# Optimization experiments

Hardware: AMD Instinct MI355X
Metric: run time of the kernel (lower is better)

Reference implementation:

```python
import jax, jax.numpy as jnp
import numpy as np

B, S, H = 2, 4096, 1024
NKH, NVH, DK, DV = 8, 16, 64, 64
KEY_DIM = NKH * DK
VAL_DIM = NVH * DV
CONV_DIM = 2 * KEY_DIM + VAL_DIM
KSZ = 4
EPS = 1e-6


def setup_inputs() -> dict:
    key = jax.random.key(0)
    ks = jax.random.split(key, 8)
    s = 0.02
    return {
        "hidden_states": jax.random.normal(ks[0], (B, S, H), jnp.float32),
        "W_qkv": jax.random.normal(ks[1], (CONV_DIM, H), jnp.float32) * s,
        "conv_w": jax.random.normal(ks[2], (CONV_DIM, 1, KSZ), jnp.float32) * 0.1,
        "W_z": jax.random.normal(ks[3], (VAL_DIM, H), jnp.float32) * s,
        "W_b": jax.random.normal(ks[4], (NVH, H), jnp.float32) * s,
        "W_a": jax.random.normal(ks[5], (NVH, H), jnp.float32) * s,
        "dt_bias": jnp.ones((NVH,), jnp.float32),
        "A_log": jnp.log(jax.random.uniform(ks[6], (NVH,), jnp.float32, 0.1, 16.0)),
        "norm_weight": jnp.ones((DV,), jnp.float32),
        "W_out": jax.random.normal(ks[7], (H, VAL_DIM), jnp.float32) * s,
    }


def _forward(hidden_states, W_qkv, conv_w, W_z, W_b, W_a, dt_bias, A_log, norm_weight, W_out):
    b, s, _ = hidden_states.shape
    # fused qkv projection -> depthwise causal conv -> silu
    mixed = hidden_states @ W_qkv.T                       # [b,s,conv_dim]
    x = mixed.transpose(0, 2, 1)                          # [b,conv_dim,s]
    y = jax.lax.conv_general_dilated(
        x, conv_w, (1,), [(KSZ - 1, 0)],
        dimension_numbers=("NCH", "OIH", "NCH"),
        feature_group_count=CONV_DIM)                     # causal: left pad k-1
    mixed = jax.nn.silu(y).transpose(0, 2, 1)             # [b,s,conv_dim]

    z = (hidden_states @ W_z.T).reshape(b, s, NVH, DV)
    beta = jax.nn.sigmoid(hidden_states @ W_b.T)          # [b,s,nvh]
    a = hidden_states @ W_a.T
    g = -jnp.exp(A_log) * jax.nn.softplus(a + dt_bias)    # [b,s,nvh]

    q, k, v = jnp.split(mixed, [KEY_DIM, 2 * KEY_DIM], axis=-1)
    q = q.reshape(b, s, NKH, DK)
    k = k.reshape(b, s, NKH, DK)
    v = v.reshape(b, s, NVH, DV)
    rep = NVH // NKH
    if rep > 1:  # GQA: repeat_interleave along head dim
        q = jnp.repeat(q, rep, axis=2)
        k = jnp.repeat(k, rep, axis=2)
    q = q * (DK ** -0.5)

    # gated delta-rule recurrence over time (state: [b,h,dk,dv])
    def step(Sst, inp):
        q_t, k_t, v_t, g_t, b_t = inp                     # [b,h,dk],[b,h,dk],[b,h,dv],[b,h],[b,h]
        Sst = Sst * jnp.exp(g_t)[..., None, None]
        kv = jnp.einsum("bhkv,bhk->bhv", Sst, k_t)
        delta = (v_t - kv) * b_t[..., None]
        Sst = Sst + k_t[..., None] * delta[..., None, :]
        o = jnp.einsum("bhkv,bhk->bhv", Sst, q_t)
        return Sst, o

    S0 = jnp.zeros((b, NVH, DK, DV), jnp.float32)
    xs = (q.transpose(1, 0, 2, 3), k.transpose(1, 0, 2, 3), v.transpose(1, 0, 2, 3),
          g.transpose(1, 0, 2), beta.transpose(1, 0, 2))
    _, o = jax.lax.scan(step, S0, xs)                     # o: [s,b,h,dv]
    o = o.transpose(1, 0, 2, 3)                           # [b,s,h,dv]

    # gated RMSNorm over head_v_dim: x * silu(z), rmsnorm, * weight
    h_ = o * jax.nn.silu(z)
    var = jnp.mean(h_ * h_, axis=-1, keepdims=True)
    h_ = h_ * jax.lax.rsqrt(var + EPS) * norm_weight

    return h_.reshape(b, s, VAL_DIM) @ W_out.T            # [b,s,hidden]


def reference(hidden_states, W_qkv, conv_w, W_z, W_b, W_a, dt_bias, A_log, norm_weight, W_out):
    return _forward(hidden_states, W_qkv, conv_w, W_z, W_b, W_a, dt_bias, A_log, norm_weight, W_out)
```

## Files before the change

### kernel.cpp

```cpp
#include <hip/hip_runtime.h>
#include <hip/hip_bf16.h>
#include <stdint.h>

#define B_    2
#define S_    4096
#define H_    1024
#define NKH_  8
#define NVH_  16
#define DK_   64
#define DV_   64
#define KEYD_ 512
#define CDIM_ 2048
#define VALD_ 1024
#define NCHUNK_ 64
#define CS_   64

using bf16 = __hip_bfloat16;
using bf16x8 = __attribute__((ext_vector_type(8))) short;
using f32x4  = __attribute__((ext_vector_type(4))) float;

__device__ inline float bsh2f(short s) {
  union { ushort u; bf16 h; } c; c.u = (ushort)s; return __bfloat162float(c.h);
}
__device__ inline short f2bsh(float f) {
  union { ushort u; bf16 h; } c; c.h = __float2bfloat16(f); return (short)c.u;
}

__device__ __forceinline__ void gload16(const bf16* g, short* lds) {
  __builtin_amdgcn_global_load_lds(
      (const __attribute__((address_space(1))) void*)g,
      (__attribute__((address_space(3))) void*)lds, 16, 0, 0);
}

__global__ __launch_bounds__(256) void castf2b(const float* __restrict__ x,
                                               bf16* __restrict__ y, long n) {
  const long i = ((long)blockIdx.x * 256 + threadIdx.x) * 4;
  if (i >= n) return;
  float4 v = *(const float4*)(x + i);
  union { ushort4 u; bf16 h[4]; } o;
  o.h[0] = __float2bfloat16(v.x);
  o.h[1] = __float2bfloat16(v.y);
  o.h[2] = __float2bfloat16(v.z);
  o.h[3] = __float2bfloat16(v.w);
  *(ushort4*)(y + i) = o.u;
}

template <typename OT>
__global__ __launch_bounds__(256) void gemm_bt(const bf16* __restrict__ A,
                                               const bf16* __restrict__ Bm,
                                               OT* __restrict__ C,
                                               int M, int N, int K) {
  __shared__ short Asm[128 * 32];
  __shared__ short Bsm[128 * 32];
  const int t = threadIdx.x;
  const int w = t >> 6, l = t & 63;
  const int ntn = N >> 7;
  const int bm = blockIdx.x / ntn, bn = blockIdx.x % ntn;
  const int m0 = bm << 7, n0 = bn << 7;
  const int wm = (w >> 1) << 6, wn = (w & 1) << 6;

  f32x4 acc[4][4] = {};

  const int grow = l >> 2;
  const int gc8 = (l & 3) << 3;
  const bf16* Agl = A + (long)m0 * K + gc8;
  const bf16* Bgl = Bm + (long)n0 * K + gc8;

  const int lm = l & 15;
  const int kk = (l >> 4) << 3;
  const short* ar0 = &Asm[(wm + lm) * 32 + kk];
  const short* br0 = &Bsm[(wn + lm) * 32 + kk];

  for (int k0 = 0; k0 < K; k0 += 32) {
    __syncthreads();
#pragma unroll
    for (int j = 0; j < 2; ++j) {
      const int s = w * 2 + j;
      gload16(Agl + (long)(s * 16 + grow) * K + k0, &Asm[s * 16 * 32]);
      gload16(Bgl + (long)(s * 16 + grow) * K + k0, &Bsm[s * 16 * 32]);
    }
    __syncthreads();
    bf16x8 af[4], bfr[4];
#pragma unroll
    for (int mi = 0; mi < 4; ++mi) af[mi] = *(const bf16x8*)(ar0 + mi * 16 * 32);
#pragma unroll
    for (int ni = 0; ni < 4; ++ni) bfr[ni] = *(const bf16x8*)(br0 + ni * 16 * 32);
#pragma unroll
    for (int mi = 0; mi < 4; ++mi)
#pragma unroll
      for (int ni = 0; ni < 4; ++ni)
        acc[mi][ni] = __builtin_amdgcn_mfma_f32_16x16x32_bf16(af[mi], bfr[ni],
                                                              acc[mi][ni], 0, 0, 0);
  }

  const int r0 = (l >> 4) << 2;
  const int cn = l & 15;
#pragma unroll
  for (int mi = 0; mi < 4; ++mi)
#pragma unroll
    for (int ni = 0; ni < 4; ++ni) {
      long base = (long)(m0 + wm + mi * 16 + r0) * N + (n0 + wn + ni * 16 + cn);
#pragma unroll
      for (int r = 0; r < 4; ++r) {
        if constexpr (sizeof(OT) == 2)
          C[base + (long)r * N] = __float2bfloat16(acc[mi][ni][r]);
        else
          C[base + (long)r * N] = acc[mi][ni][r];
      }
    }
}

__global__ __launch_bounds__(256) void conv3(const bf16* __restrict__ mixed,
                                             const float* __restrict__ cw,
                                             bf16* __restrict__ qkv) {
  const long idx = (long)blockIdx.x * 256 + threadIdx.x;
  const int c0 = (int)(idx & 255) << 3;
  const long row = idx >> 8;
  const int s = (int)(row & (S_ - 1));

  bf16x8 mv[4];
#pragma unroll
  for (int j = 0; j < 4; ++j) {
    if (s - 3 + j >= 0)
      mv[j] = *(const bf16x8*)(mixed + (row + j - 3) * CDIM_ + c0);
    else
      mv[j] = (bf16x8){0, 0, 0, 0, 0, 0, 0, 0};
  }

  const float qs = (c0 < KEYD_) ? 0.125f : 1.f;
  union { ushort4 u4[2]; short h[8]; } o;
#pragma unroll
  for (int e = 0; e < 8; ++e) {
    const float4 w = *(const float4*)(cw + (c0 + e) * 4);
    float acc = 0.f;
    acc = fmaf(w.x, bsh2f(mv[0][e]), acc);
    acc = fmaf(w.y, bsh2f(mv[1][e]), acc);
    acc = fmaf(w.z, bsh2f(mv[2][e]), acc);
    acc = fmaf(w.w, bsh2f(mv[3][e]), acc);
    const float y = qs * (acc / (1.f + __expf(-acc)));
    o.h[e] = f2bsh(y);
  }
  *(bf16x8*)((uint16_t*)qkv + row * CDIM_ + c0) = *(bf16x8*)&o.h[0];
}

__global__ __launch_bounds__(256) void proj_ba2(const float* __restrict__ hs,
                                                const float* __restrict__ Wb,
                                                const float* __restrict__ Wa,
                                                const float* __restrict__ dtb,
                                                const float* __restrict__ Alog,
                                                float* __restrict__ beta,
                                                float* __restrict__ g) {
  __shared__ float4 hrow[8][257];
  const long row0 = (long)blockIdx.x * 8;
  const int tid = threadIdx.x;
  for (int i = tid; i < 2048; i += 256) {
    const int r = i >> 8, c4 = i & 255;
    hrow[r][c4] = *(const float4*)(hs + (row0 + r) * H_ + (long)c4 * 4);
  }
  __syncthreads();
  const int j = tid >> 3, r = tid & 7;
  const float4* Wp = (const float4*)(j < 16 ? Wb + (long)j * H_
                                            : Wa + (long)(j - 16) * H_);
  float4 a4 = {0.f, 0.f, 0.f, 0.f};
#pragma unroll 4
  for (int i = 0; i < 256; ++i) {
    const float4 w = Wp[i];
    const float4 hv = hrow[r][i];
    a4.x = fmaf(w.x, hv.x, a4.x);
    a4.y = fmaf(w.y, hv.y, a4.y);
    a4.z = fmaf(w.z, hv.z, a4.z);
    a4.w = fmaf(w.w, hv.w, a4.w);
  }
  const float acc = (a4.x + a4.y) + (a4.z + a4.w);
  const long row = row0 + r;
  if (j < 16) {
    beta[row * NVH_ + j] = 1.f / (1.f + __expf(-acc));
  } else {
    const int hh = j - 16;
    const float x = acc + dtb[hh];
    const float sp = (x > 20.f) ? x : log1pf(__expf(x));
    g[row * NVH_ + hh] = -__expf(Alog[hh]) * sp;
  }
}

__global__ __launch_bounds__(256) void chunk_pre(const bf16* __restrict__ qkv,
                                                 const float* __restrict__ beta,
                                                 const float* __restrict__ g,
                                                 bf16* __restrict__ Wws,
                                                 bf16* __restrict__ U0ws,
                                                 float* __restrict__ lgws,
                                                 bf16* __restrict__ McT,
                                                 bf16* __restrict__ Bc) {
  __shared__ short Ksm[64][72];
  __shared__ short Vsm[64][72];
  __shared__ float Tsm[64][64];
  __shared__ short KpT[64][72];
  __shared__ float Xl[128][67];
  __shared__ float lgs[64];
  __shared__ float bts[64];
  __shared__ float belg[64];

  short (*XB)[36]   = (short (*)[36]) & Vsm[0][0];
  short (*TloB)[40] = (short (*)[40]) & Ksm[0][0];
  short (*WT)[72]   = (short (*)[72]) & Tsm[0][0];
  short (*U0T)[72]  = Vsm;

  const int blk = blockIdx.x;
  const int hb = blk & 31, c = blk >> 5;
  const long task = (long)hb * 64 + c;
  const int h = hb & 15, b = hb >> 4, kh = h >> 1;
  const long t0 = (long)b * S_ + (long)c * CS_;
  const int tid = threadIdx.x;
  const int wv = tid >> 6, l = tid & 63;
  const int lm = l & 15, lk8 = (l >> 4) << 3;
  const int r0 = (l >> 4) << 2, cn = l & 15;
  const int srow = tid >> 2, scol = (tid & 3) * 16;

  {
    const bf16* kp = qkv + (t0 + srow) * CDIM_ + KEYD_ + kh * 64 + scol;
    const bf16* vp = qkv + (t0 + srow) * CDIM_ + 2 * KEYD_ + h * 64 + scol;
    *(bf16x8*)&Ksm[srow][scol]     = *(const bf16x8*)(kp);
    *(bf16x8*)&Ksm[srow][scol + 8] = *(const bf16x8*)(kp + 8);
    *(bf16x8*)&Vsm[srow][scol]     = *(const bf16x8*)(vp);
    *(bf16x8*)&Vsm[srow][scol + 8] = *(const bf16x8*)(vp + 8);
  }
  if (tid < 64) {
    bts[tid] = beta[(t0 + tid) * NVH_ + h];
    lgs[tid] = g[(t0 + tid) * NVH_ + h];
  }
  __syncthreads();

  if (tid < 64) {
    float x = lgs[tid];
#pragma unroll
    for (int d = 1; d < 64; d <<= 1) {
      const float y = __shfl_up(x, d);
      if (tid >= d) x += y;
    }
    lgs[tid] = x;
    belg[tid] = bts[tid] * __expf(x);
  }
  __syncthreads();

  if (tid < 128) {
    f32x4 acc[2][4] = {};
#pragma unroll
    for (int ks = 0; ks < 2; ++ks) {
      bf16x8 bfr[4];
#pragma unroll
      for (int ni = 0; ni < 4; ++ni)
        bfr[ni] = *(const bf16x8*)&Ksm[ni * 16 + lm][lk8 + ks * 32];
#pragma unroll
      for (int mi = 0; mi < 2; ++mi) {
        bf16x8 afr = *(const bf16x8*)&Ksm[(wv * 2 + mi) * 16 + lm][lk8 + ks * 32];
#pragma unroll
        for (int ni = 0; ni < 4; ++ni)
          acc[mi][ni] = __builtin_amdgcn_mfma_f32_16x16x32_bf16(afr, bfr[ni],
                                                                acc[mi][ni], 0, 0, 0);
      }
    }
#pragma unroll
    for (int mi = 0; mi < 2; ++mi)
#pragma unroll
      for (int ni = 0; ni < 4; ++ni)
#pragma unroll
        for (int r = 0; r < 4; ++r) {
          const int t = (wv * 2 + mi) * 16 + r0 + r;
          const int i = ni * 16 + cn;
          Tsm[t][i] = (i < t) ? bts[t] * __expf(lgs[t] - lgs[i]) * acc[mi][ni][r]
                              : 0.f;
        }
  } else {
    const int idx = tid - 128;
    const int tt = idx >> 1;
    const int o2 = (idx & 1) * 32;
    const float dec = __expf(lgs[63] - lgs[tt]);
#pragma unroll 8
    for (int k = 0; k < 32; ++k)
      KpT[o2 + k][tt] = f2bsh(dec * bsh2f(Ksm[tt][o2 + k]));
  }
  __syncthreads();

  auto solve32 = [&](int base) {
    for (int j = base; j < base + 32; j += 8) {
      float xs[8];
#pragma unroll
      for (int a = 0; a < 8; ++a) xs[a] = Xl[tid][j + a];
#pragma unroll
      for (int a = 1; a < 8; ++a)
#pragma unroll
        for (int bb = 0; bb < a; ++bb)
          xs[a] = fmaf(-Tsm[j + a][j + bb], xs[bb], xs[a]);
#pragma unroll
      for (int a = 1; a < 8; ++a) Xl[tid][j + a] = xs[a];
      const int tend = base + 32;
#pragma unroll 2
      for (int tt = j + 8; tt < tend; ++tt) {
        const float4 ta = *(const float4*)&Tsm[tt][j];
        const float4 tb = *(const float4*)&Tsm[tt][j + 4];
        float v = Xl[tid][tt];
        v = fmaf(-ta.x, xs[0], v); v = fmaf(-ta.y, xs[1], v);
        v = fmaf(-ta.z, xs[2], v); v = fmaf(-ta.w, xs[3], v);
        v = fmaf(-tb.x, xs[4], v); v = fmaf(-tb.y, xs[5], v);
        v = fmaf(-tb.z, xs[6], v); v = fmaf(-tb.w, xs[7], v);
        Xl[tid][tt] = v;
      }
    }
  };

  if (tid < 128) {
    const int colW = tid & 63;
    const bool isW = tid < 64;
#pragma unroll 8
    for (int t = 0; t < CS_; ++t)
      Xl[tid][t] = isW ? belg[t] * bsh2f(Ksm[t][colW])
                       : bts[t] * bsh2f(Vsm[t][colW]);
    solve32(0);
  }
  if (tid < 64) lgws[task * 64 + tid] = lgs[tid];
  __syncthreads();

  {
    const int col = tid & 127, uh = (tid >> 7) * 16;
#pragma unroll
    for (int u = 0; u < 16; ++u)
      XB[col][uh + u] = f2bsh(Xl[col][uh + u]);
  }
  if (tid < 128) {
    const int m = tid >> 2, u0 = (tid & 3) * 8;
#pragma unroll
    for (int u = 0; u < 8; ++u)
      TloB[m][u0 + u] = f2bsh(Tsm[32 + m][u0 + u]);
  }
  __syncthreads();

  {
#pragma unroll
    for (int ni2 = 0; ni2 < 2; ++ni2) {
      const int ni = wv * 2 + ni2;
      bf16x8 bfr = *(const bf16x8*)&XB[ni * 16 + lm][lk8];
#pragma unroll
      for (int mi = 0; mi < 2; ++mi) {
        bf16x8 afr = *(const bf16x8*)&TloB[mi * 16 + lm][lk8];
        f32x4 uacc = {};
        uacc = __builtin_amdgcn_mfma_f32_16x16x32_bf16(afr, bfr, uacc, 0, 0, 0);
#pragma unroll
        for (int r = 0; r < 4; ++r)
          Xl[ni * 16 + cn][32 + mi * 16 + r0 + r] -= uacc[r];
      }
    }
  }
  __syncthreads();

  if (tid < 128) solve32(32);
  __syncthreads();

  if (tid < 128) {
    const int colW = tid & 63;
    const bool isW = tid < 64;
    bf16* dst = (isW ? Wws : U0ws) + task * 4096 + colW;
    short (*XT)[72] = isW ? WT : U0T;
#pragma unroll 4
    for (int t = 0; t < CS_; t += 2) {
      const float v0 = Xl[tid][t], v1 = Xl[tid][t + 1];
      dst[(long)t * 64] = __float2bfloat16(v0);
      dst[(long)(t + 1) * 64] = __float2bfloat16(v1);
      short2 pk; pk.x = f2bsh(v0); pk.y = f2bsh(v1);
      *(short2*)&XT[colW][t] = pk;
    }
  }
  __syncthreads();

  {
    f32x4 macc[4] = {};
#pragma unroll
    for (int ks = 0; ks < 2; ++ks) {
      bf16x8 afr = *(const bf16x8*)&KpT[wv * 16 + lm][lk8 + ks * 32];
#pragma unroll
      for (int ni = 0; ni < 4; ++ni) {
        bf16x8 bfr = *(const bf16x8*)&WT[ni * 16 + lm][lk8 + ks * 32];
        macc[ni] = __builtin_amdgcn_mfma_f32_16x16x32_bf16(afr, bfr, macc[ni], 0, 0, 0);
      }
    }
#pragma unroll
    for (int ni = 0; ni < 4; ++ni)
#pragma unroll
      for (int r = 0; r < 4; ++r)
        McT[task * 4096 + (wv * 16 + r0 + r) * 64 + ni * 16 + cn] =
            __float2bfloat16(-macc[ni][r]);
  }
  {
    f32x4 bacc[4] = {};
#pragma unroll
    for (int ks = 0; ks < 2; ++ks) {
      bf16x8 afr = *(const bf16x8*)&U0T[wv * 16 + lm][lk8 + ks * 32];
#pragma unroll
      for (int ni = 0; ni < 4; ++ni) {
        bf16x8 bfr = *(const bf16x8*)&KpT[ni * 16 + lm][lk8 + ks * 32];
        bacc[ni] = __builtin_amdgcn_mfma_f32_16x16x32_bf16(afr, bfr, bacc[ni], 0, 0, 0);
      }
    }
#pragma unroll
    for (int ni = 0; ni < 4; ++ni)
#pragma unroll
      for (int r = 0; r < 4; ++r)
        Bc[task * 4096 + (wv * 16 + r0 + r) * 64 + ni * 16 + cn] =
            __float2bfloat16(bacc[ni][r]);
  }
}

__global__ __launch_bounds__(256) void chunk_state(const bf16* __restrict__ McT,
                                                   const bf16* __restrict__ Bc,
                                                   const float* __restrict__ lgws,
                                                   bf16* __restrict__ Sb) {
  __shared__ short Msm[2][4][64][72];
  __shared__ short Bsm[2][4][64][72];
  __shared__ short Ssm[64][72];
  __shared__ float lgsm[2][4];

  const int hb = blockIdx.x;
  const int tid = threadIdx.x, wv = tid >> 6, l = tid & 63;
  const int lm = l & 15, lk8 = (l >> 4) << 3;
  const int r0 = (l >> 4) << 2, cn = l & 15;
  const int srow = tid >> 2, scol = (tid & 3) * 16;

  for (int i = tid; i < 64 * 72; i += 256) ((short*)Ssm)[i] = 0;
  f32x4 Sreg[4] = {};

  bf16x8 mr0[4], mr1[4], br0[4], br1[4];
  float lgn0, lgn1, lgn2, lgn3;

  auto gload = [&](int g) {
#pragma unroll
    for (int cc = 0; cc < 4; ++cc) {
      const long tt = (long)hb * 64 + g * 4 + cc;
      const bf16* mp = McT + tt * 4096 + srow * 64 + scol;
      const bf16* bp = Bc + tt * 4096 + srow * 64 + scol;
      mr0[cc] = *(const bf16x8*)(mp);
      mr1[cc] = *(const bf16x8*)(mp + 8);
      br0[cc] = *(const bf16x8*)(bp);
      br1[cc] = *(const bf16x8*)(bp + 8);
    }
    const long tb = (long)hb * 64 + g * 4;
    lgn0 = lgws[(tb + 0) * 64 + 63];
    lgn1 = lgws[(tb + 1) * 64 + 63];
    lgn2 = lgws[(tb + 2) * 64 + 63];
    lgn3 = lgws[(tb + 3) * 64 + 63];
  };
  auto lwrite = [&](int g) {
    const int bu = g & 1;
#pragma unroll
    for (int cc = 0; cc < 4; ++cc) {
      *(bf16x8*)&Msm[bu][cc][srow][scol]     = mr0[cc];
      *(bf16x8*)&Msm[bu][cc][srow][scol + 8] = mr1[cc];
      *(bf16x8*)&Bsm[bu][cc][srow][scol]     = br0[cc];
      *(bf16x8*)&Bsm[bu][cc][srow][scol + 8] = br1[cc];
    }
    if (tid == 0) {
      lgsm[bu][0] = lgn0; lgsm[bu][1] = lgn1;
      lgsm[bu][2] = lgn2; lgsm[bu][3] = lgn3;
    }
  };

  gload(0);
  lwrite(0);
  gload(1);
  __syncthreads();

  for (int g = 0; g < 16; ++g) {
    const int bu = g & 1;
    if (g + 1 < 16) lwrite(g + 1);
    if (g + 2 < 16) gload(g + 2);
#pragma unroll
    for (int cc = 0; cc < 4; ++cc) {
      const int c = g * 4 + cc;
      {
        bf16* sp = Sb + ((long)hb * 64 + c) * 4096;
#pragma unroll
        for (int ni = 0; ni < 4; ++ni)
#pragma unroll
          for (int r = 0; r < 4; ++r)
            sp[(wv * 16 + r0 + r) * 64 + ni * 16 + cn] = __float2bfloat16(Sreg[ni][r]);
      }
      bf16x8 sfr0 = *(const bf16x8*)&Ssm[wv * 16 + lm][lk8];
      bf16x8 sfr1 = *(const bf16x8*)&Ssm[wv * 16 + lm][lk8 + 32];
      f32x4 kacc[4] = {};
#pragma unroll
      for (int ni = 0; ni < 4; ++ni) {
        bf16x8 b0 = *(const bf16x8*)&Msm[bu][cc][ni * 16 + lm][lk8];
        kacc[ni] = __builtin_amdgcn_mfma_f32_16x16x32_bf16(sfr0, b0, kacc[ni], 0, 0, 0);
        bf16x8 b1 = *(const bf16x8*)&Msm[bu][cc][ni * 16 + lm][lk8 + 32];
        kacc[ni] = __builtin_amdgcn_mfma_f32_16x16x32_bf16(sfr1, b1, kacc[ni], 0, 0, 0);
      }
      const float eend = __expf(lgsm[bu][cc]);
#pragma unroll
      for (int ni = 0; ni < 4; ++ni)
#pragma unroll
        for (int r = 0; r < 4; ++r) {
          const float bv = bsh2f(Bsm[bu][cc][wv * 16 + r0 + r][ni * 16 + cn]);
          Sreg[ni][r] = eend * Sreg[ni][r] + kacc[ni][r] + bv;
          Ssm[wv * 16 + r0 + r][ni * 16 + cn] = f2bsh(Sreg[ni][r]);
        }
    }
    __syncthreads();
  }
}

__global__ __launch_bounds__(256) void chunk_out(const bf16* __restrict__ qkv,
                                                 const bf16* __restrict__ Wws,
                                                 const bf16* __restrict__ U0ws,
                                                 const float* __restrict__ lgws,
                                                 const bf16* __restrict__ Sb,
                                                 float* __restrict__ o) {
  __shared__ short Qsm[64][72];
  __shared__ short Ksm[64][72];
  __shared__ short Wsm[64][72];
  __shared__ short Usm[64][72];
  __shared__ short Amm[64][72];
  __shared__ short Dsm[64][72];
  __shared__ float lgs[64];

  const int blk = blockIdx.x;
  const int hb = blk & 31, c = blk >> 5;
  const long task = (long)hb * 64 + c;
  const int h = hb & 15, b = hb >> 4, kh = h >> 1;
  const long sb = (long)b * S_ + (long)c * CS_;
  const int tid = threadIdx.x, wv = tid >> 6, l = tid & 63;
  const int lm = l & 15, lk8 = (l >> 4) << 3;
  const int r0 = (l >> 4) << 2, cn = l & 15;
  const int srow = tid >> 2, scol = (tid & 3) * 16;

  const bf16* sp = Sb + task * 4096 + (wv * 16 + lm) * 64 + lk8;
  bf16x8 sfr0 = *(const bf16x8*)(sp);
  bf16x8 sfr1 = *(const bf16x8*)(sp + 32);

  {
    const bf16* qp = qkv + (sb + srow) * CDIM_ + kh * 64 + scol;
    const bf16* kp = qkv + (sb + srow) * CDIM_ + KEYD_ + kh * 64 + scol;
    const bf16* wp = Wws + task * 4096 + srow * 64 + scol;
    const bf16* up = U0ws + task * 4096 + srow * 64 + scol;
    *(bf16x8*)&Qsm[srow][scol]     = *(const bf16x8*)(qp);
    *(bf16x8*)&Qsm[srow][scol + 8] = *(const bf16x8*)(qp + 8);
    *(bf16x8*)&Ksm[srow][scol]     = *(const bf16x8*)(kp);
    *(bf16x8*)&Ksm[srow][scol + 8] = *(const bf16x8*)(kp + 8);
    *(bf16x8*)&Wsm[srow][scol]     = *(const bf16x8*)(wp);
    *(bf16x8*)&Wsm[srow][scol + 8] = *(const bf16x8*)(wp + 8);
    *(bf16x8*)&Usm[srow][scol]     = *(const bf16x8*)(up);
    *(bf16x8*)&Usm[srow][scol + 8] = *(const bf16x8*)(up + 8);
    if (tid < 64) lgs[tid] = lgws[task * 64 + tid];
  }
  __syncthreads();

  {
    f32x4 aacc[4] = {};
#pragma unroll
    for (int ks = 0; ks < 2; ++ks) {
      bf16x8 qa = *(const bf16x8*)&Qsm[wv * 16 + lm][lk8 + ks * 32];
#pragma unroll
      for (int ni = 0; ni < 4; ++ni) {
        bf16x8 kb = *(const bf16x8*)&Ksm[ni * 16 + lm][lk8 + ks * 32];
        aacc[ni] = __builtin_amdgcn_mfma_f32_16x16x32_bf16(qa, kb, aacc[ni], 0, 0, 0);
      }
    }
#pragma unroll
    for (int ni = 0; ni < 4; ++ni)
#pragma unroll
      for (int r = 0; r < 4; ++r) {
        const int t = wv * 16 + r0 + r, i = ni * 16 + cn;
        Amm[t][i] = f2bsh((i <= t) ? aacc[ni][r] * __expf(lgs[t] - lgs[i]) : 0.f);
      }
  }
  __syncthreads();

  {
    const float sc = __expf(lgs[srow]);
#pragma unroll
    for (int j = 0; j < 16; ++j)
      Qsm[srow][scol + j] = f2bsh(sc * bsh2f(Qsm[srow][scol + j]));
  }
  __syncthreads();

  {
    f32x4 dacc[4] = {};
#pragma unroll
    for (int ni = 0; ni < 4; ++ni) {
      bf16x8 w0 = *(const bf16x8*)&Wsm[ni * 16 + lm][lk8];
      dacc[ni] = __builtin_amdgcn_mfma_f32_16x16x32_bf16(sfr0, w0, dacc[ni], 0, 0, 0);
      bf16x8 w1 = *(const bf16x8*)&Wsm[ni * 16 + lm][lk8 + 32];
      dacc[ni] = __builtin_amdgcn_mfma_f32_16x16x32_bf16(sfr1, w1, dacc[ni], 0, 0, 0);
    }
#pragma unroll
    for (int ni = 0; ni < 4; ++ni)
#pragma unroll
      for (int r = 0; r < 4; ++r) {
        const int t = ni * 16 + cn, v = r0 + r;
        Dsm[wv * 16 + v][t] = f2bsh(bsh2f(Usm[t][wv * 16 + v]) - dacc[ni][r]);
      }
  }
  bf16x8 dfr0 = *(const bf16x8*)&Dsm[wv * 16 + lm][lk8];
  bf16x8 dfr1 = *(const bf16x8*)&Dsm[wv * 16 + lm][lk8 + 32];

  {
    f32x4 oacc[4] = {};
#pragma unroll
    for (int mi = 0; mi < 4; ++mi) {
      bf16x8 q0 = *(const bf16x8*)&Qsm[mi * 16 + lm][lk8];
      oacc[mi] = __builtin_amdgcn_mfma_f32_16x16x32_bf16(q0, sfr0, oacc[mi], 0, 0, 0);
      bf16x8 q1 = *(const bf16x8*)&Qsm[mi * 16 + lm][lk8 + 32];
      oacc[mi] = __builtin_amdgcn_mfma_f32_16x16x32_bf16(q1, sfr1, oacc[mi], 0, 0, 0);
    }
#pragma unroll
    for (int mi = 0; mi < 4; ++mi) {
      bf16x8 a0 = *(const bf16x8*)&Amm[mi * 16 + lm][lk8];
      oacc[mi] = __builtin_amdgcn_mfma_f32_16x16x32_bf16(a0, dfr0, oacc[mi], 0, 0, 0);
      bf16x8 a1 = *(const bf16x8*)&Amm[mi * 16 + lm][lk8 + 32];
      oacc[mi] = __builtin_amdgcn_mfma_f32_16x16x32_bf16(a1, dfr1, oacc[mi], 0, 0, 0);
    }
#pragma unroll
    for (int mi = 0; mi < 4; ++mi)
#pragma unroll
      for (int r = 0; r < 4; ++r) {
        const int t = mi * 16 + r0 + r;
        o[(sb + t) * VALD_ + h * 64 + wv * 16 + cn] = oacc[mi][r];
      }
  }
}

__global__ __launch_bounds__(256) void gnorm3(const float* __restrict__ o,
                                              const float* __restrict__ z,
                                              const float* __restrict__ nw,
                                              bf16* __restrict__ hn) {
  const long idx = (long)blockIdx.x * 256 + threadIdx.x;
  const float* op = o + idx * 64;
  const float* zp = z + idx * 64;
  float4 hv[16];
  float ss = 0.f;
#pragma unroll
  for (int i = 0; i < 16; ++i) {
    const float4 ov = *(const float4*)(op + i * 4);
    const float4 zv = *(const float4*)(zp + i * 4);
    float4 h;
    h.x = ov.x * (zv.x / (1.f + __expf(-zv.x)));
    h.y = ov.y * (zv.y / (1.f + __expf(-zv.y)));
    h.z = ov.z * (zv.z / (1.f + __expf(-zv.z)));
    h.w = ov.w * (zv.w / (1.f + __expf(-zv.w)));
    hv[i] = h;
    ss = fmaf(h.x, h.x, ss); ss = fmaf(h.y, h.y, ss);
    ss = fmaf(h.z, h.z, ss); ss = fmaf(h.w, h.w, ss);
  }
  const float r = rsqrtf(ss * (1.f / 64.f) + 1e-6f);
#pragma unroll
  for (int i = 0; i < 16; i += 2) {
    const float4 w0 = *(const float4*)(nw + i * 4);
    const float4 w1 = *(const float4*)(nw + i * 4 + 4);
    bf16x8 pk;
    pk[0] = f2bsh(hv[i].x * r * w0.x);     pk[1] = f2bsh(hv[i].y * r * w0.y);
    pk[2] = f2bsh(hv[i].z * r * w0.z);     pk[3] = f2bsh(hv[i].w * r * w0.w);
    pk[4] = f2bsh(hv[i + 1].x * r * w1.x); pk[5] = f2bsh(hv[i + 1].y * r * w1.y);
    pk[6] = f2bsh(hv[i + 1].z * r * w1.z); pk[7] = f2bsh(hv[i + 1].w * r * w1.w);
    *(bf16x8*)((uint16_t*)hn + idx * 64 + i * 4) = pk;
  }
}

extern "C" void kernel_launch(void* const* d_in, const int* in_sizes, int n_in,
                              void* d_out, int out_size, void* d_ws, size_t ws_size,
                              hipStream_t stream) {
  float* out = (float*)d_out;
  const int M = B_ * S_;

  int ih, iqkv, icw, iz, ib, ia, idtb, ialog, inw, iout;
  if (n_in >= 10 && in_sizes[0] == 8388608) {
    ih = 0; iqkv = 1; icw = 2; iz = 3; ib = 4; ia = 5;
    idtb = 6; ialog = 7; inw = 8; iout = 9;
  } else {
    ih = iqkv = icw = iz = ib = ia = idtb = ialog = inw = iout = -1;
    for (int i = 0; i < n_in; ++i) {
      switch (in_sizes[i]) {
        case 8388608: ih = i; break;
        case 2097152: iqkv = i; break;
        case 8192:    icw = i; break;
        case 64:      inw = i; break;
        case 1048576: if (iz < 0) iz = i; else iout = i; break;
        case 16384:   if (ib < 0) ib = i; else ia = i; break;
        case 16:      if (idtb < 0) idtb = i; else ialog = i; break;
        default: break;
      }
    }
  }
  const float* hs   = (const float*)d_in[ih];
  const float* Wqkv = (const float*)d_in[iqkv];
  const float* cw   = (const float*)d_in[icw];
  const float* Wz   = (const float*)d_in[iz];
  const float* Wb   = (const float*)d_in[ib];
  const float* Wa   = (const float*)d_in[ia];
  const float* dtb  = (const float*)d_in[idtb];
  const float* Alog = (const float*)d_in[ialog];
  const float* nwv  = (const float*)d_in[inw];
  const float* Wout = (const float*)d_in[iout];

  char* p = (char*)d_ws;
  bf16*  mixed = (bf16*)p;
  float* of    = (float*)p;
  bf16*  McTw  = (bf16*)p;
  bf16*  Bcw   = (bf16*)(p + (size_t)2048 * 4096 * 2);
  p += (size_t)M * CDIM_ * 2;
  bf16*  hs_b  = (bf16*)p;
  bf16*  qkvb  = (bf16*)p;
  bf16*  hn    = (bf16*)p; p += (size_t)M * CDIM_ * 2;
  bf16*  Wqkv_b= (bf16*)p; p += (size_t)CDIM_ * H_ * 2;
  bf16*  Wz_b  = (bf16*)p; p += (size_t)H_ * H_ * 2;
  bf16*  Wout_b= (bf16*)p; p += (size_t)H_ * H_ * 2;
  float* betaf = (float*)p; p += (size_t)M * NVH_ * 4;
  float* gf    = (float*)p; p += (size_t)M * NVH_ * 4;
  bf16*  Wws   = (bf16*)p; p += (size_t)2048 * 4096 * 2;
  bf16*  U0ws  = (bf16*)p; p += (size_t)2048 * 4096 * 2;
  float* lgws  = (float*)p; p += (size_t)2048 * 64 * 4;
  bf16*  Sbw   = (bf16*)p; p += (size_t)2048 * 4096 * 2;
  float* zb    = out;

  {
    long n;
    n = (long)M * H_;     castf2b<<<(int)(n / 4 / 256), 256, 0, stream>>>(hs,   hs_b,   n);
    n = (long)CDIM_ * H_; castf2b<<<(int)(n / 4 / 256), 256, 0, stream>>>(Wqkv, Wqkv_b, n);
    n = (long)H_ * H_;    castf2b<<<(int)(n / 4 / 256), 256, 0, stream>>>(Wz,   Wz_b,   n);
    n = (long)H_ * H_;    castf2b<<<(int)(n / 4 / 256), 256, 0, stream>>>(Wout, Wout_b, n);
  }
  gemm_bt<bf16><<<(M / 128) * (CDIM_ / 128), 256, 0, stream>>>(hs_b, Wqkv_b, mixed, M, CDIM_, H_);
  gemm_bt<float><<<(M / 128) * (H_ / 128), 256, 0, stream>>>(hs_b, Wz_b, zb, M, H_, H_);
  proj_ba2<<<M / 8, 256, 0, stream>>>(hs, Wb, Wa, dtb, Alog, betaf, gf);
  conv3<<<(int)(((long)M * CDIM_) / 8 / 256), 256, 0, stream>>>(mixed, cw, qkvb);
  chunk_pre<<<2048, 256, 0, stream>>>(qkvb, betaf, gf, Wws, U0ws, lgws, McTw, Bcw);
  chunk_state<<<32, 256, 0, stream>>>(McTw, Bcw, lgws, Sbw);
  chunk_out<<<2048, 256, 0, stream>>>(qkvb, Wws, U0ws, lgws, Sbw, of);
  gnorm3<<<(M * NVH_) / 256, 256, 0, stream>>>(of, zb, nwv, hn);
  gemm_bt<float><<<(M / 128) * (H_ / 128), 256, 0, stream>>>(hn, Wout_b, out, M, H_, H_);
}
```

Before: 477.8 us.

## Keep chunk_pre triangular-solve columns in registers instead of shared memory

The 128x67 float shared buffer used for the per-column forward substitution in chunk_pre is replaced by a per-thread 64-float register array. The solve loops are fully unrolled, and the MFMA correction term is passed through a bf16 shared scratch that aliases existing buffers. Dropping about 34 KB of LDS together with __launch_bounds__(256,3) is meant to let more blocks reside per CU. In exchange, register pressure rises, the correction is now rounded to bf16 before it is subtracted, and the partially unrolled store loop indexes the register array dynamically, which could push it to scratch memory.

Result: slower. 509.0 us (+6.5%).

```diff
diff --git a/kernel.cpp b/kernel.cpp
--- a/kernel.cpp
+++ b/kernel.cpp
@@ -183,25 +183,25 @@
   }
 }
 
-__global__ __launch_bounds__(256) void chunk_pre(const bf16* __restrict__ qkv,
-                                                 const float* __restrict__ beta,
-                                                 const float* __restrict__ g,
-                                                 bf16* __restrict__ Wws,
-                                                 bf16* __restrict__ U0ws,
-                                                 float* __restrict__ lgws,
-                                                 bf16* __restrict__ McT,
-                                                 bf16* __restrict__ Bc) {
+__global__ __launch_bounds__(256, 3) void chunk_pre(const bf16* __restrict__ qkv,
+                                                    const float* __restrict__ beta,
+                                                    const float* __restrict__ g,
+                                                    bf16* __restrict__ Wws,
+                                                    bf16* __restrict__ U0ws,
+                                                    float* __restrict__ lgws,
+                                                    bf16* __restrict__ McT,
+                                                    bf16* __restrict__ Bc) {
   __shared__ short Ksm[64][72];
   __shared__ short Vsm[64][72];
   __shared__ float Tsm[64][64];
   __shared__ short KpT[64][72];
-  __shared__ float Xl[128][67];
   __shared__ float lgs[64];
   __shared__ float bts[64];
   __shared__ float belg[64];
 
   short (*XB)[36]   = (short (*)[36]) & Vsm[0][0];
   short (*TloB)[40] = (short (*)[40]) & Ksm[0][0];
+  short (*UcrB)[68] = (short (*)[68]) & Ksm[0][0];
   short (*WT)[72]   = (short (*)[72]) & Tsm[0][0];
   short (*U0T)[72]  = Vsm;
 
@@ -281,59 +281,64 @@
   }
   __syncthreads();
 
-  auto solve32 = [&](int base) {
-    for (int j = base; j < base + 32; j += 8) {
+  float x[64];
+  const int colW = tid & 63;
+  const bool isW = tid < 64;
+
+  auto solve32 = [&](const int base) {
+#pragma unroll
+    for (int jj = 0; jj < 32; jj += 8) {
+      const int j = base + jj;
       float xs[8];
 #pragma unroll
-      for (int a = 0; a < 8; ++a) xs[a] = Xl[tid][j + a];
+      for (int a = 0; a < 8; ++a) xs[a] = x[j + a];
 #pragma unroll
       for (int a = 1; a < 8; ++a)
 #pragma unroll
         for (int bb = 0; bb < a; ++bb)
           xs[a] = fmaf(-Tsm[j + a][j + bb], xs[bb], xs[a]);
 #pragma unroll
-      for (int a = 1; a < 8; ++a) Xl[tid][j + a] = xs[a];
-      const int tend = base + 32;
-#pragma unroll 2
-      for (int tt = j + 8; tt < tend; ++tt) {
+      for (int a = 1; a < 8; ++a) x[j + a] = xs[a];
+#pragma unroll
+      for (int t2 = jj + 8; t2 < 32; ++t2) {
+        const int tt = base + t2;
         const float4 ta = *(const float4*)&Tsm[tt][j];
         const float4 tb = *(const float4*)&Tsm[tt][j + 4];
-        float v = Xl[tid][tt];
+        float v = x[tt];
         v = fmaf(-ta.x, xs[0], v); v = fmaf(-ta.y, xs[1], v);
         v = fmaf(-ta.z, xs[2], v); v = fmaf(-ta.w, xs[3], v);
         v = fmaf(-tb.x, xs[4], v); v = fmaf(-tb.y, xs[5], v);
         v = fmaf(-tb.z, xs[6], v); v = fmaf(-tb.w, xs[7], v);
-        Xl[tid][tt] = v;
+        x[tt] = v;
       }
     }
   };
 
   if (tid < 128) {
-    const int colW = tid & 63;
-    const bool isW = tid < 64;
-#pragma unroll 8
+#pragma unroll
     for (int t = 0; t < CS_; ++t)
-      Xl[tid][t] = isW ? belg[t] * bsh2f(Ksm[t][colW])
-                       : bts[t] * bsh2f(Vsm[t][colW]);
+      x[t] = isW ? belg[t] * bsh2f(Ksm[t][colW])
+                 : bts[t] * bsh2f(Vsm[t][colW]);
     solve32(0);
   }
   if (tid < 64) lgws[task * 64 + tid] = lgs[tid];
   __syncthreads();
 
-  {
-    const int col = tid & 127, uh = (tid >> 7) * 16;
-#pragma unroll
-    for (int u = 0; u < 16; ++u)
-      XB[col][uh + u] = f2bsh(Xl[col][uh + u]);
-  }
   if (tid < 128) {
-    const int m = tid >> 2, u0 = (tid & 3) * 8;
+#pragma unroll
+    for (int p = 0; p < 16; ++p) {
+      short2 pk; pk.x = f2bsh(x[2 * p]); pk.y = f2bsh(x[2 * p + 1]);
+      *(short2*)&XB[tid][2 * p] = pk;
+    }
+  } else {
+    const int m = (tid - 128) >> 2, u0 = (tid & 3) * 8;
 #pragma unroll
     for (int u = 0; u < 8; ++u)
       TloB[m][u0 + u] = f2bsh(Tsm[32 + m][u0 + u]);
   }
   __syncthreads();
 
+  f32x4 uacc2[2][2] = {};
   {
 #pragma unroll
     for (int ni2 = 0; ni2 < 2; ++ni2) {
@@ -342,30 +347,38 @@
 #pragma unroll
       for (int mi = 0; mi < 2; ++mi) {
         bf16x8 afr = *(const bf16x8*)&TloB[mi * 16 + lm][lk8];
-        f32x4 uacc = {};
-        uacc = __builtin_amdgcn_mfma_f32_16x16x32_bf16(afr, bfr, uacc, 0, 0, 0);
-#pragma unroll
-        for (int r = 0; r < 4; ++r)
-          Xl[ni * 16 + cn][32 + mi * 16 + r0 + r] -= uacc[r];
-      }
-    }
-  }
-  __syncthreads();
-
-  if (tid < 128) solve32(32);
+        uacc2[ni2][mi] = __builtin_amdgcn_mfma_f32_16x16x32_bf16(afr, bfr,
+                                                                 uacc2[ni2][mi], 0, 0, 0);
+      }
+    }
+  }
+  __syncthreads();
+
+#pragma unroll
+  for (int ni2 = 0; ni2 < 2; ++ni2)
+#pragma unroll
+    for (int mi = 0; mi < 2; ++mi)
+#pragma unroll
+      for (int r = 0; r < 4; ++r)
+        UcrB[mi * 16 + r0 + r][wv * 32 + ni2 * 16 + cn] = f2bsh(uacc2[ni2][mi][r]);
   __syncthreads();
 
   if (tid < 128) {
-    const int colW = tid & 63;
-    const bool isW = tid < 64;
+#pragma unroll
+    for (int i = 0; i < 32; ++i)
+      x[32 + i] -= bsh2f(UcrB[i][tid]);
+    solve32(32);
+  }
+  __syncthreads();
+
+  if (tid < 128) {
     bf16* dst = (isW ? Wws : U0ws) + task * 4096 + colW;
     short (*XT)[72] = isW ? WT : U0T;
 #pragma unroll 4
     for (int t = 0; t < CS_; t += 2) {
-      const float v0 = Xl[tid][t], v1 = Xl[tid][t + 1];
-      dst[(long)t * 64] = __float2bfloat16(v0);
-      dst[(long)(t + 1) * 64] = __float2bfloat16(v1);
-      short2 pk; pk.x = f2bsh(v0); pk.y = f2bsh(v1);
+      dst[(long)t * 64] = __float2bfloat16(x[t]);
+      dst[(long)(t + 1) * 64] = __float2bfloat16(x[t + 1]);
+      short2 pk; pk.x = f2bsh(x[t]); pk.y = f2bsh(x[t + 1]);
       *(short2*)&XT[colW][t] = pk;
     }
   }
```
